# Kernel tuning notes

Measured on AMD Instinct MI355X. Metric: run time of the kernel, lower is better.

The kernel has to match this reference:

```python
import jax, jax.numpy as jnp
import numpy as np

# LeViT-style Attention, linear (use_conv=False) path, eval-mode BatchNorm.
B, N, DIM = 32, 784, 512
H, KD, VD, RES = 8, 32, 128, 28          # num_heads, key_dim, val_dim, resolution
QKV_OUT = H * (2 * KD + VD)              # 1536
VAL_ATTN = H * VD                        # 1024
EPS = 1e-5


def _bn(x, g, b, m, v):
    # BatchNorm1d (eval): affine normalize over channel dim (last axis)
    return (x - m) * (g * jax.lax.rsqrt(v + EPS)) + b


def _rel_pos_idxs(res):
    pos = np.stack(np.meshgrid(np.arange(res), np.arange(res), indexing='ij')).reshape(2, -1)
    rel = np.abs(pos[:, :, None] - pos[:, None, :])
    return jnp.asarray(rel[0] * res + rel[1], dtype=jnp.int32)  # (N, N)


def setup_inputs() -> dict:
    key = jax.random.key(0)
    ks = jax.random.split(key, 8)
    x = jax.random.normal(ks[0], (B, N, DIM), jnp.float32)
    qkv_w = jax.random.normal(ks[1], (QKV_OUT, DIM), jnp.float32) * 0.02
    qkv_g = jnp.ones((QKV_OUT,), jnp.float32)
    qkv_b = jnp.zeros((QKV_OUT,), jnp.float32)
    qkv_m = jax.random.normal(ks[2], (QKV_OUT,), jnp.float32) * 0.1
    qkv_v = jax.random.uniform(ks[3], (QKV_OUT,), jnp.float32, 0.5, 1.5)
    ab = jax.random.normal(ks[4], (H, RES * RES), jnp.float32) * 0.02
    idxs = _rel_pos_idxs(RES)
    proj_w = jax.random.normal(ks[5], (DIM, VAL_ATTN), jnp.float32) * 0.02
    proj_g = jnp.ones((DIM,), jnp.float32)   # bn_weight_init=0 in torch; use 1 for nontrivial grads
    proj_b = jnp.zeros((DIM,), jnp.float32)
    proj_m = jax.random.normal(ks[6], (DIM,), jnp.float32) * 0.1
    proj_v = jax.random.uniform(ks[7], (DIM,), jnp.float32, 0.5, 1.5)
    return {"x": x, "qkv_w": qkv_w, "qkv_g": qkv_g, "qkv_b": qkv_b, "qkv_m": qkv_m,
            "qkv_v": qkv_v, "ab": ab, "proj_w": proj_w, "proj_g": proj_g,
            "proj_b": proj_b, "proj_m": proj_m, "proj_v": proj_v, "idxs": idxs}


def reference(x, qkv_w, qkv_g, qkv_b, qkv_m, qkv_v, ab,
              proj_w, proj_g, proj_b, proj_m, proj_v, idxs):
    b, n, _ = x.shape
    scale = KD ** -0.5
    # fused QKV projection (Linear no bias) + BatchNorm1d
    qkv = _bn(jnp.einsum('bnc,oc->bno', x, qkv_w), qkv_g, qkv_b, qkv_m, qkv_v)
    qkv = qkv.reshape(b, n, H, 2 * KD + VD)
    q, k, v = jnp.split(qkv, [KD, 2 * KD], axis=3)  # (b,n,H,KD/KD/VD)
    bias = ab[:, idxs]                               # (H, N, N) relative-position bias
    attn = jnp.einsum('bnhd,bmhd->bhnm', q, k) * scale + bias
    attn = jax.nn.softmax(attn, axis=-1)
    o = jnp.einsum('bhnm,bmhd->bnhd', attn, v).reshape(b, n, VAL_ATTN)
    # proj: Hardswish -> Linear -> BN
    o = o * jax.nn.relu6(o + 3.0) * (1.0 / 6.0)
    out = _bn(jnp.einsum('bnk,ok->bno', o, proj_w), proj_g, proj_b, proj_m, proj_v)
    return out
```

## Files before the change

kernel.cpp:

```cpp
#include <hip/hip_runtime.h>
#include <hip/hip_bf16.h>

#define NB 32
#define NN 784
#define NNP 896
#define DIMC 512
#define NH 8
#define KD 32
#define VD 128
#define QKV_OUT 1536
#define VAL_ATTN 1024
#define PROW 136
#define KROW 40

typedef __attribute__((ext_vector_type(4))) float floatx4;
typedef __attribute__((ext_vector_type(8))) short shortx8;
typedef __attribute__((ext_vector_type(4))) unsigned short ushortx4;
typedef __attribute__((ext_vector_type(4))) unsigned int uintx4;
typedef unsigned short ushort_t;

__device__ __forceinline__ unsigned short f2bf(float f) {
    union { float f; unsigned int u; } v; v.f = f;
    unsigned int r = v.u + 0x7fffu + ((v.u >> 16) & 1u);
    return (unsigned short)(r >> 16);
}
__device__ __forceinline__ float bf2f(unsigned short s) {
    union { unsigned int u; float f; } v; v.u = ((unsigned int)s) << 16;
    return v.f;
}
__device__ __forceinline__ void gld16(void* lds, const void* g) {
    __builtin_amdgcn_global_load_lds((const __attribute__((address_space(1))) void*)g,
                                     (__attribute__((address_space(3))) void*)lds, 16, 0, 0);
}

__global__ void cvt_bf16(const float* __restrict__ in, ushort_t* __restrict__ out, int n4) {
    int i = blockIdx.x * 256 + threadIdx.x;
    if (i < n4) {
        floatx4 f = ((const floatx4*)in)[i];
        ushortx4 u;
        #pragma unroll
        for (int j = 0; j < 4; ++j) u[j] = f2bf(f[j]);
        ((ushortx4*)out)[i] = u;
    }
}

__global__ void bn_prep(const float* __restrict__ g, const float* __restrict__ b,
                        const float* __restrict__ m, const float* __restrict__ v,
                        float* __restrict__ scale, float* __restrict__ shift, int n) {
    int i = blockIdx.x * 256 + threadIdx.x;
    if (i < n) {
        float s = g[i] * rsqrtf(v[i] + 1e-5f);
        scale[i] = s;
        shift[i] = b[i] - m[i] * s;
    }
}

__global__ void bias_prep(const float* __restrict__ ab, const int* __restrict__ idxs,
                          ushort_t* __restrict__ bias) {
    int tid = blockIdx.x * 256 + threadIdx.x;
    if (tid >= NH * NN * NNP) return;
    int j = tid % NNP;
    int rest = tid / NNP;
    int i = rest % NN;
    int h = rest / NN;
    float v = -30000.0f;
    if (j < NN) v = ab[h * NN + idxs[i * NN + j]];
    bias[tid] = f2bf(v);
}

__global__ __launch_bounds__(256, 2)
void qkv_gemm(const ushort_t* __restrict__ xb, const ushort_t* __restrict__ wb,
              const float* __restrict__ scale, const float* __restrict__ shift,
              ushort_t* __restrict__ qbuf, ushort_t* __restrict__ kbuf,
              ushort_t* __restrict__ vbuf) {
    __shared__ ushort_t As[128 * 32];
    __shared__ ushort_t Bs[128 * 32];
    const int t = threadIdx.x;
    const int m0 = blockIdx.x * 128;
    const int n0 = blockIdx.y * 128;
    const int wave = t >> 6, lane = t & 63;
    const int wm = wave >> 1, wn = wave & 1;
    const int l16 = lane & 15, quad = lane >> 4;
    const int r4 = lane >> 2, c8 = lane & 3;

    floatx4 acc[4][4] = {};

    const ushort_t* agp = xb + (size_t)(m0 + wave * 16 + r4) * DIMC + c8 * 8;
    const ushort_t* bgp = wb + (size_t)(n0 + wave * 16 + r4) * DIMC + c8 * 8;
    ushort_t* alp = As + wave * 16 * 32;
    ushort_t* blp = Bs + wave * 16 * 32;

    for (int k0 = 0; k0 < DIMC; k0 += 32) {
        gld16(alp,           agp + k0);
        gld16(alp + 64 * 32, agp + (size_t)64 * DIMC + k0);
        gld16(blp,           bgp + k0);
        gld16(blp + 64 * 32, bgp + (size_t)64 * DIMC + k0);
        __syncthreads();
        shortx8 af[4], bfr[4];
        #pragma unroll
        for (int i = 0; i < 4; ++i)
            af[i] = *(const shortx8*)(As + (wm * 64 + i * 16 + l16) * 32 + quad * 8);
        #pragma unroll
        for (int j = 0; j < 4; ++j)
            bfr[j] = *(const shortx8*)(Bs + (wn * 64 + j * 16 + l16) * 32 + quad * 8);
        #pragma unroll
        for (int i = 0; i < 4; ++i)
            #pragma unroll
            for (int j = 0; j < 4; ++j)
                acc[i][j] = __builtin_amdgcn_mfma_f32_16x16x32_bf16(af[i], bfr[j], acc[i][j], 0, 0, 0);
        __syncthreads();
    }

    #pragma unroll
    for (int j = 0; j < 4; ++j) {
        const int gn = n0 + wn * 64 + j * 16 + l16;
        const float sc = scale[gn], sh = shift[gn];
        const int h = gn / 192, rr = gn % 192;
        if (rr < 2 * KD) {
            #pragma unroll
            for (int i = 0; i < 4; ++i) {
                #pragma unroll
                for (int r = 0; r < 4; ++r) {
                    const int gm = m0 + wm * 64 + i * 16 + quad * 4 + r;
                    const int bb = gm / NN, n = gm - bb * NN;
                    const ushort_t bv = f2bf(acc[i][j][r] * sc + sh);
                    const size_t bh = (size_t)bb * NH + h;
                    if (rr < KD) qbuf[(bh * NN + n) * KD + rr] = bv;
                    else         kbuf[(bh * NNP + n) * KD + (rr - KD)] = bv;
                }
            }
        } else {
            const int d = rr - 2 * KD;
            #pragma unroll
            for (int i = 0; i < 4; ++i) {
                const int gm0 = m0 + wm * 64 + i * 16 + quad * 4;
                const int bb = gm0 / NN, n = gm0 - bb * NN;
                const size_t bh = (size_t)bb * NH + h;
                ushortx4 pk;
                #pragma unroll
                for (int r = 0; r < 4; ++r) pk[r] = f2bf(acc[i][j][r] * sc + sh);
                *(ushortx4*)(vbuf + (bh * VD + d) * NNP + n) = pk;
            }
        }
    }
}

__global__ __launch_bounds__(256, 4)
void attn_kernel(const ushort_t* __restrict__ qbuf, const ushort_t* __restrict__ kbuf,
                 const ushort_t* __restrict__ vbuf, const ushort_t* __restrict__ bias,
                 ushort_t* __restrict__ obuf) {
    __shared__ ushort_t Ks[128 * KROW];
    __shared__ ushort_t Ps[64 * PROW];
    __shared__ float linv[64];

    const int t = threadIdx.x;
    const int wave = t >> 6, lane = t & 63;
    const int l16 = lane & 15, quad = lane >> 4;
    const int bid = blockIdx.x;
    const int b = bid & 31;
    const int hq = bid >> 5;
    const int h = hq & 7;
    const int qt = hq >> 3;
    const int bh = b * NH + h;
    const int i0 = qt * 64;
    const int mvalid = min(4, (NN - i0 + 15) >> 4);
    const bool swave = wave < mvalid;
    const float scale = 0.17677669529663687f;

    const ushort_t* qbase = qbuf + ((size_t)bh * NN + i0) * KD;
    const ushort_t* kbase = kbuf + (size_t)bh * NNP * KD;
    const ushort_t* vbase = vbuf + (size_t)bh * VD * NNP;
    const ushort_t* bbase = bias + ((size_t)h * NN + i0) * NNP;

    shortx8 qf = {};
    if (swave) qf = *(const shortx8*)(qbase + (wave * 16 + l16) * KD + quad * 8);

    float lacc[4] = {0.f, 0.f, 0.f, 0.f};
    floatx4 oacc[4][2] = {};

    const int srow = t >> 2, sq4 = t & 3;

    for (int c = 0; c < 7; ++c) {
        #pragma unroll
        for (int rr = 0; rr < 2; ++rr) {
            const int row = rr * 64 + srow;
            *(uintx4*)(Ks + row * KROW + sq4 * 8) =
                *(const uintx4*)(kbase + (size_t)(c * 128 + row) * KD + sq4 * 8);
        }
        __syncthreads();

        if (swave) {
            #pragma unroll
            for (int jt = 0; jt < 8; ++jt) {
                shortx8 kf = *(const shortx8*)(Ks + (jt * 16 + l16) * KROW + quad * 8);
                floatx4 d = {};
                d = __builtin_amdgcn_mfma_f32_16x16x32_bf16(qf, kf, d, 0, 0, 0);
                const int j = c * 128 + jt * 16 + l16;
                #pragma unroll
                for (int r = 0; r < 4; ++r) {
                    const int lr = wave * 16 + quad * 4 + r;
                    const float bv = bf2f(bbase[(size_t)lr * NNP + j]);
                    const float e = __expf(d[r] * scale + bv);
                    lacc[r] += e;
                    Ps[lr * PROW + jt * 16 + l16] = f2bf(e);
                }
            }
        }
        __syncthreads();

        {
            const ushort_t* vb = vbase + (size_t)(wave * 32) * NNP + c * 128;
            #pragma unroll
            for (int ks = 0; ks < 4; ++ks) {
                shortx8 v0 = *(const shortx8*)(vb + (size_t)l16 * NNP + ks * 32 + quad * 8);
                shortx8 v1 = *(const shortx8*)(vb + (size_t)(16 + l16) * NNP + ks * 32 + quad * 8);
                #pragma unroll
                for (int ms = 0; ms < 4; ++ms) {
                    if (ms < mvalid) {
                        shortx8 af = *(const shortx8*)(Ps + (ms * 16 + l16) * PROW + ks * 32 + quad * 8);
                        oacc[ms][0] = __builtin_amdgcn_mfma_f32_16x16x32_bf16(af, v0, oacc[ms][0], 0, 0, 0);
                        oacc[ms][1] = __builtin_amdgcn_mfma_f32_16x16x32_bf16(af, v1, oacc[ms][1], 0, 0, 0);
                    }
                }
            }
        }
    }

    if (swave) {
        #pragma unroll
        for (int r = 0; r < 4; ++r) {
            float s = lacc[r];
            s += __shfl_xor(s, 1, 16);
            s += __shfl_xor(s, 2, 16);
            s += __shfl_xor(s, 4, 16);
            s += __shfl_xor(s, 8, 16);
            if (l16 == r) linv[wave * 16 + quad * 4 + r] = 1.0f / s;
        }
    }
    __syncthreads();

    #pragma unroll
    for (int ms = 0; ms < 4; ++ms) {
        if (ms < mvalid) {
            #pragma unroll
            for (int vt = 0; vt < 2; ++vt) {
                const int vd = h * VD + wave * 32 + vt * 16 + l16;
                #pragma unroll
                for (int r = 0; r < 4; ++r) {
                    const int row = i0 + ms * 16 + quad * 4 + r;
                    const float o = oacc[ms][vt][r] * linv[ms * 16 + quad * 4 + r];
                    const float hs = o * fminf(fmaxf(o + 3.0f, 0.0f), 6.0f) * (1.0f / 6.0f);
                    obuf[((size_t)b * NN + row) * VAL_ATTN + vd] = f2bf(hs);
                }
            }
        }
    }
}

__global__ __launch_bounds__(256, 2)
void proj_gemm(const ushort_t* __restrict__ obuf, const ushort_t* __restrict__ pwb,
               const float* __restrict__ pscale, const float* __restrict__ pshift,
               float* __restrict__ out) {
    __shared__ ushort_t As[128 * 32];
    __shared__ ushort_t Bs[128 * 32];
    const int t = threadIdx.x;
    const int m0 = blockIdx.x * 128;
    const int n0 = blockIdx.y * 128;
    const int wave = t >> 6, lane = t & 63;
    const int wm = wave >> 1, wn = wave & 1;
    const int l16 = lane & 15, quad = lane >> 4;
    const int r4 = lane >> 2, c8 = lane & 3;

    floatx4 acc[4][4] = {};

    const ushort_t* agp = obuf + (size_t)(m0 + wave * 16 + r4) * VAL_ATTN + c8 * 8;
    const ushort_t* bgp = pwb + (size_t)(n0 + wave * 16 + r4) * VAL_ATTN + c8 * 8;
    ushort_t* alp = As + wave * 16 * 32;
    ushort_t* blp = Bs + wave * 16 * 32;

    for (int k0 = 0; k0 < VAL_ATTN; k0 += 32) {
        gld16(alp,           agp + k0);
        gld16(alp + 64 * 32, agp + (size_t)64 * VAL_ATTN + k0);
        gld16(blp,           bgp + k0);
        gld16(blp + 64 * 32, bgp + (size_t)64 * VAL_ATTN + k0);
        __syncthreads();
        shortx8 af[4], bfr[4];
        #pragma unroll
        for (int i = 0; i < 4; ++i)
            af[i] = *(const shortx8*)(As + (wm * 64 + i * 16 + l16) * 32 + quad * 8);
        #pragma unroll
        for (int j = 0; j < 4; ++j)
            bfr[j] = *(const shortx8*)(Bs + (wn * 64 + j * 16 + l16) * 32 + quad * 8);
        #pragma unroll
        for (int i = 0; i < 4; ++i)
            #pragma unroll
            for (int j = 0; j < 4; ++j)
                acc[i][j] = __builtin_amdgcn_mfma_f32_16x16x32_bf16(af[i], bfr[j], acc[i][j], 0, 0, 0);
        __syncthreads();
    }

    #pragma unroll
    for (int j = 0; j < 4; ++j) {
        const int gn = n0 + wn * 64 + j * 16 + l16;
        const float sc = pscale[gn], sh = pshift[gn];
        #pragma unroll
        for (int i = 0; i < 4; ++i) {
            #pragma unroll
            for (int r = 0; r < 4; ++r) {
                const int gm = m0 + wm * 64 + i * 16 + quad * 4 + r;
                out[(size_t)gm * DIMC + gn] = acc[i][j][r] * sc + sh;
            }
        }
    }
}

extern "C" void kernel_launch(void* const* d_in, const int* in_sizes, int n_in,
                              void* d_out, int out_size, void* d_ws, size_t ws_size,
                              hipStream_t stream) {
    const float* x      = (const float*)d_in[0];
    const float* qkv_w  = (const float*)d_in[1];
    const float* qkv_g  = (const float*)d_in[2];
    const float* qkv_b  = (const float*)d_in[3];
    const float* qkv_m  = (const float*)d_in[4];
    const float* qkv_v  = (const float*)d_in[5];
    const float* ab     = (const float*)d_in[6];
    const float* proj_w = (const float*)d_in[7];
    const float* proj_g = (const float*)d_in[8];
    const float* proj_b = (const float*)d_in[9];
    const float* proj_m = (const float*)d_in[10];
    const float* proj_v = (const float*)d_in[11];
    const int*   idxs   = (const int*)d_in[12];
    float* out = (float*)d_out;

    char* ws = (char*)d_ws;
    size_t off = 0;
    auto alloc = [&](size_t bytes) {
        void* p = ws + off;
        off = (off + bytes + 255) & ~(size_t)255;
        return p;
    };
    ushort_t* qbuf = (ushort_t*)alloc((size_t)NB * NH * NN * KD * 2);
    ushort_t* kbuf = (ushort_t*)alloc((size_t)NB * NH * NNP * KD * 2);
    ushort_t* vbuf = (ushort_t*)alloc((size_t)NB * NH * VD * NNP * 2);
    ushort_t* obuf = (ushort_t*)alloc((size_t)NB * NN * VAL_ATTN * 2);
    ushort_t* bias = (ushort_t*)alloc((size_t)NH * NN * NNP * 2);
    ushort_t* xb   = (ushort_t*)alloc((size_t)NB * NN * DIMC * 2);
    ushort_t* wqb  = (ushort_t*)alloc((size_t)QKV_OUT * DIMC * 2);
    ushort_t* pwb  = (ushort_t*)alloc((size_t)DIMC * VAL_ATTN * 2);
    float* qscale = (float*)alloc(QKV_OUT * 4);
    float* qshift = (float*)alloc(QKV_OUT * 4);
    float* pscale = (float*)alloc(DIMC * 4);
    float* pshift = (float*)alloc(DIMC * 4);

    const int nx4 = NB * NN * DIMC / 4;
    const int nw4 = QKV_OUT * DIMC / 4;
    const int np4 = DIMC * VAL_ATTN / 4;
    cvt_bf16<<<(nx4 + 255) / 256, 256, 0, stream>>>(x, xb, nx4);
    cvt_bf16<<<(nw4 + 255) / 256, 256, 0, stream>>>(qkv_w, wqb, nw4);
    cvt_bf16<<<(np4 + 255) / 256, 256, 0, stream>>>(proj_w, pwb, np4);
    bn_prep<<<6, 256, 0, stream>>>(qkv_g, qkv_b, qkv_m, qkv_v, qscale, qshift, QKV_OUT);
    bn_prep<<<2, 256, 0, stream>>>(proj_g, proj_b, proj_m, proj_v, pscale, pshift, DIMC);
    bias_prep<<<(NH * NN * NNP + 255) / 256, 256, 0, stream>>>(ab, idxs, bias);
    qkv_gemm<<<dim3(196, 12), 256, 0, stream>>>(xb, wqb, qscale, qshift, qbuf, kbuf, vbuf);
    attn_kernel<<<dim3(32 * NH * 13), 256, 0, stream>>>(qbuf, kbuf, vbuf, bias, obuf);
    proj_gemm<<<dim3(196, 4), 256, 0, stream>>>(obuf, pwb, pscale, pshift, out);
}
```

Measured before the change: 406.2 us.

## Transpose QK MFMA, prefetch K tiles in registers, use exp2 with prescaled bias

The QK^T MFMA now runs with K as the A operand, so each lane holds four consecutive key columns of one query row. That allows vectorized bias loads and vectorized P stores, and the row-sum reduction drops to two shuffles. K tiles are staged one tile ahead through registers, and the sync order is rearranged so the global K load overlaps compute. Softmax uses exp2f with the bias prescaled by log2(e) and a merged scale constant, removing a multiply per element. Launch-bound occupancy hints are raised on all three kernels, which may force register spilling.

```diff
diff --git a/kernel.cpp b/kernel.cpp
--- a/kernel.cpp
+++ b/kernel.cpp
@@ -63,12 +63,12 @@
     int rest = tid / NNP;
     int i = rest % NN;
     int h = rest / NN;
-    float v = -30000.0f;
-    if (j < NN) v = ab[h * NN + idxs[i * NN + j]];
+    float v = -43000.0f;
+    if (j < NN) v = 1.4426950408889634f * ab[h * NN + idxs[i * NN + j]];
     bias[tid] = f2bf(v);
 }
 
-__global__ __launch_bounds__(256, 2)
+__global__ __launch_bounds__(256, 4)
 void qkv_gemm(const ushort_t* __restrict__ xb, const ushort_t* __restrict__ wb,
               const float* __restrict__ scale, const float* __restrict__ shift,
               ushort_t* __restrict__ qbuf, ushort_t* __restrict__ kbuf,
@@ -145,7 +145,7 @@
     }
 }
 
-__global__ __launch_bounds__(256, 4)
+__global__ __launch_bounds__(256, 5)
 void attn_kernel(const ushort_t* __restrict__ qbuf, const ushort_t* __restrict__ kbuf,
                  const ushort_t* __restrict__ vbuf, const ushort_t* __restrict__ bias,
                  ushort_t* __restrict__ obuf) {
@@ -165,7 +165,7 @@
     const int i0 = qt * 64;
     const int mvalid = min(4, (NN - i0 + 15) >> 4);
     const bool swave = wave < mvalid;
-    const float scale = 0.17677669529663687f;
+    const float SC2 = 0.25505679f;
 
     const ushort_t* qbase = qbuf + ((size_t)bh * NN + i0) * KD;
     const ushort_t* kbase = kbuf + (size_t)bh * NNP * KD;
@@ -175,38 +175,54 @@
     shortx8 qf = {};
     if (swave) qf = *(const shortx8*)(qbase + (wave * 16 + l16) * KD + quad * 8);
 
-    float lacc[4] = {0.f, 0.f, 0.f, 0.f};
+    float lacc = 0.0f;
     floatx4 oacc[4][2] = {};
 
     const int srow = t >> 2, sq4 = t & 3;
+    const ushort_t* kstage = kbase + (size_t)srow * KD + sq4 * 8;
+    ushort_t* kdst0 = Ks + srow * KROW + sq4 * 8;
+    ushort_t* kdst1 = Ks + (64 + srow) * KROW + sq4 * 8;
+
+    uintx4 kr0 = *(const uintx4*)(kstage);
+    uintx4 kr1 = *(const uintx4*)(kstage + (size_t)64 * KD);
+    *(uintx4*)kdst0 = kr0;
+    *(uintx4*)kdst1 = kr1;
+    kr0 = *(const uintx4*)(kstage + (size_t)128 * KD);
+    kr1 = *(const uintx4*)(kstage + (size_t)192 * KD);
+    __syncthreads();
+
+    const int myrow = wave * 16 + l16;
+    const ushort_t* brow = bbase + (size_t)myrow * NNP + quad * 4;
+    ushort_t* prow = Ps + myrow * PROW + quad * 4;
 
     for (int c = 0; c < 7; ++c) {
-        #pragma unroll
-        for (int rr = 0; rr < 2; ++rr) {
-            const int row = rr * 64 + srow;
-            *(uintx4*)(Ks + row * KROW + sq4 * 8) =
-                *(const uintx4*)(kbase + (size_t)(c * 128 + row) * KD + sq4 * 8);
-        }
-        __syncthreads();
-
         if (swave) {
             #pragma unroll
-            for (int jt = 0; jt < 8; ++jt) {
-                shortx8 kf = *(const shortx8*)(Ks + (jt * 16 + l16) * KROW + quad * 8);
+            for (int kt = 0; kt < 8; ++kt) {
+                shortx8 kf = *(const shortx8*)(Ks + (kt * 16 + l16) * KROW + quad * 8);
                 floatx4 d = {};
-                d = __builtin_amdgcn_mfma_f32_16x16x32_bf16(qf, kf, d, 0, 0, 0);
-                const int j = c * 128 + jt * 16 + l16;
+                d = __builtin_amdgcn_mfma_f32_16x16x32_bf16(kf, qf, d, 0, 0, 0);
+                ushortx4 bv = *(const ushortx4*)(brow + c * 128 + kt * 16);
+                ushortx4 pv;
                 #pragma unroll
                 for (int r = 0; r < 4; ++r) {
-                    const int lr = wave * 16 + quad * 4 + r;
-                    const float bv = bf2f(bbase[(size_t)lr * NNP + j]);
-                    const float e = __expf(d[r] * scale + bv);
-                    lacc[r] += e;
-                    Ps[lr * PROW + jt * 16 + l16] = f2bf(e);
+                    const float e = exp2f(fmaf(d[r], SC2, bf2f(bv[r])));
+                    lacc += e;
+                    pv[r] = f2bf(e);
                 }
-            }
-        }
-        __syncthreads();
+                *(ushortx4*)(prow + kt * 16) = pv;
+            }
+        }
+        __syncthreads();
+
+        if (c < 6) {
+            *(uintx4*)kdst0 = kr0;
+            *(uintx4*)kdst1 = kr1;
+            if (c < 5) {
+                kr0 = *(const uintx4*)(kstage + (size_t)(c + 2) * 128 * KD);
+                kr1 = *(const uintx4*)(kstage + ((size_t)(c + 2) * 128 + 64) * KD);
+            }
+        }
 
         {
             const ushort_t* vb = vbase + (size_t)(wave * 32) * NNP + c * 128;
@@ -224,18 +240,14 @@
                 }
             }
         }
+        __syncthreads();
     }
 
     if (swave) {
-        #pragma unroll
-        for (int r = 0; r < 4; ++r) {
-            float s = lacc[r];
-            s += __shfl_xor(s, 1, 16);
-            s += __shfl_xor(s, 2, 16);
-            s += __shfl_xor(s, 4, 16);
-            s += __shfl_xor(s, 8, 16);
-            if (l16 == r) linv[wave * 16 + quad * 4 + r] = 1.0f / s;
-        }
+        float s = lacc;
+        s += __shfl_xor(s, 16);
+        s += __shfl_xor(s, 32);
+        if (quad == 0) linv[myrow] = 1.0f / s;
     }
     __syncthreads();
 
@@ -257,7 +269,7 @@
     }
 }
 
-__global__ __launch_bounds__(256, 2)
+__global__ __launch_bounds__(256, 4)
 void proj_gemm(const ushort_t* __restrict__ obuf, const ushort_t* __restrict__ pwb,
                const float* __restrict__ pscale, const float* __restrict__ pshift,
                float* __restrict__ out) {
```

Measured after the change: 438.9 us. 8.0% more time.
